# Optimization experiments

Hardware: AMD Instinct MI355X
Metric: run time of the kernel (lower is better)

## Reference

```python
import jax, jax.numpy as jnp
import numpy as np

D = 256; NH = 8; DH = D // NH; NL = 4; NP = 4; DFFN = 1024
SPATIAL = [(128, 128), (64, 64), (32, 32), (16, 16)]
LEN_IN = sum(h * w for h, w in SPATIAL)
N, LQ = 8, 1000


def _ln(x, g, b, eps=1e-5):
    m = jnp.mean(x, -1, keepdims=True)
    v = jnp.mean((x - m) ** 2, -1, keepdims=True)
    return (x - m) * jax.lax.rsqrt(v + eps) * g + b


def _ms_deform_core(value, loc, attn_w):
    # value (N,Len_in,NH,DH); loc (N,Lq,NH,NL,NP,2) in [0,1]; attn_w (N,Lq,NH,NL,NP)
    n, lq = loc.shape[0], loc.shape[1]
    out = jnp.zeros((n, NH, lq, DH), value.dtype)
    start = 0
    for l, (Hl, Wl) in enumerate(SPATIAL):
        v = value[:, start:start + Hl * Wl].transpose(0, 2, 1, 3)  # (N,NH,HW,DH)
        start += Hl * Wl
        # grid_sample-style mapping, align_corners=False, zero padding
        x = loc[:, :, :, l, :, 0] * Wl - 0.5  # (N,Lq,NH,NP)
        y = loc[:, :, :, l, :, 1] * Hl - 0.5
        x0 = jnp.floor(x); y0 = jnp.floor(y)
        lx = x - x0; ly = y - y0
        x0i = x0.astype(jnp.int32); y0i = y0.astype(jnp.int32)
        acc = jnp.zeros((n, NH, lq, NP, DH), value.dtype)
        for dy, dx, w in ((0, 0, (1 - ly) * (1 - lx)), (0, 1, (1 - ly) * lx),
                          (1, 0, ly * (1 - lx)), (1, 1, ly * lx)):
            xi = x0i + dx; yi = y0i + dy
            valid = ((xi >= 0) & (xi < Wl) & (yi >= 0) & (yi < Hl)).astype(value.dtype)
            idx = jnp.clip(yi, 0, Hl - 1) * Wl + jnp.clip(xi, 0, Wl - 1)  # (N,Lq,NH,NP)
            idx = idx.transpose(0, 2, 1, 3).reshape(n, NH, lq * NP)
            g = jnp.take_along_axis(v, idx[..., None], axis=2).reshape(n, NH, lq, NP, DH)
            acc = acc + g * (w * valid).transpose(0, 2, 1, 3)[..., None]
        out = out + jnp.sum(acc * attn_w[:, :, :, l].transpose(0, 2, 1, 3)[..., None], axis=3)
    return out.transpose(0, 2, 1, 3).reshape(n, lq, D)


def setup_inputs() -> dict:
    key = jax.random.key(0)
    ks = jax.random.split(key, 16)
    s = 0.02
    inp = {
        'tgt': jax.random.normal(ks[0], (N, LQ, D), jnp.float32),
        'query_pos': jax.random.normal(ks[1], (N, LQ, D), jnp.float32),
        'reference_points': jax.random.uniform(ks[2], (N, LQ, NL, 2), jnp.float32),
        'src': jax.random.normal(ks[3], (N, LEN_IN, D), jnp.float32),
        'spatial_shapes': jnp.array(SPATIAL, jnp.int32),
        'level_start_index': jnp.array(np.cumsum([0] + [h * w for h, w in SPATIAL[:-1]]), jnp.int32),
        # self-attention
        'sa_in_w': jax.random.normal(ks[4], (3 * D, D), jnp.float32) * s,
        'sa_in_b': jnp.zeros((3 * D,), jnp.float32),
        'sa_out_w': jax.random.normal(ks[5], (D, D), jnp.float32) * s,
        'sa_out_b': jnp.zeros((D,), jnp.float32),
        'norm2_g': jnp.ones((D,), jnp.float32), 'norm2_b': jnp.zeros((D,), jnp.float32),
        # MSDeformAttn
        'off_w': jax.random.normal(ks[6], (NH * NL * NP * 2, D), jnp.float32) * s,
        'off_b': jax.random.normal(ks[7], (NH * NL * NP * 2,), jnp.float32) * s,
        'aw_w': jax.random.normal(ks[8], (NH * NL * NP, D), jnp.float32) * s,
        'aw_b': jnp.zeros((NH * NL * NP,), jnp.float32),
        'val_w': jax.random.normal(ks[9], (D, D), jnp.float32) * s,
        'val_b': jnp.zeros((D,), jnp.float32),
        'outp_w': jax.random.normal(ks[10], (D, D), jnp.float32) * s,
        'outp_b': jnp.zeros((D,), jnp.float32),
        'norm1_g': jnp.ones((D,), jnp.float32), 'norm1_b': jnp.zeros((D,), jnp.float32),
        # FFN
        'ffn_w1': jax.random.normal(ks[11], (DFFN, D), jnp.float32) * s,
        'ffn_b1': jnp.zeros((DFFN,), jnp.float32),
        'ffn_w2': jax.random.normal(ks[12], (D, DFFN), jnp.float32) * s,
        'ffn_b2': jnp.zeros((D,), jnp.float32),
        'norm3_g': jnp.ones((D,), jnp.float32), 'norm3_b': jnp.zeros((D,), jnp.float32),
    }
    return inp


def reference(tgt, query_pos, reference_points, src, spatial_shapes, level_start_index,
              sa_in_w, sa_in_b, sa_out_w, sa_out_b, norm2_g, norm2_b,
              off_w, off_b, aw_w, aw_b, val_w, val_b, outp_w, outp_b, norm1_g, norm1_b,
              ffn_w1, ffn_b1, ffn_w2, ffn_b2, norm3_g, norm3_b):
    n, lq, _ = tgt.shape
    # ---- self-attention (q = k = tgt + pos, v = tgt), eval mode (dropout off)
    qk = tgt + query_pos
    wq, wk, wv = sa_in_w[:D], sa_in_w[D:2 * D], sa_in_w[2 * D:]
    bq, bk, bv = sa_in_b[:D], sa_in_b[D:2 * D], sa_in_b[2 * D:]
    q = (qk @ wq.T + bq).reshape(n, lq, NH, DH)
    k = (qk @ wk.T + bk).reshape(n, lq, NH, DH)
    v = (tgt @ wv.T + bv).reshape(n, lq, NH, DH)
    scores = jnp.einsum('bqhd,bkhd->bhqk', q, k) / np.sqrt(DH).astype(np.float32)
    attn = jax.nn.softmax(scores, axis=-1)
    sa = jnp.einsum('bhqk,bkhd->bqhd', attn, v).reshape(n, lq, D) @ sa_out_w.T + sa_out_b
    tgt = _ln(tgt + sa, norm2_g, norm2_b)
    # ---- multi-scale deformable cross-attention
    query = tgt + query_pos
    value = (src @ val_w.T + val_b).reshape(n, LEN_IN, NH, DH)
    offsets = (query @ off_w.T + off_b).reshape(n, lq, NH, NL, NP, 2)
    aw = (query @ aw_w.T + aw_b).reshape(n, lq, NH, NL * NP)
    aw = jax.nn.softmax(aw, axis=-1).reshape(n, lq, NH, NL, NP)
    # offset normalizer: (W_l, H_l)
    norm = jnp.stack([spatial_shapes[:, 1], spatial_shapes[:, 0]], -1).astype(tgt.dtype)
    loc = reference_points[:, :, None, :, None, :] + offsets / norm[None, None, None, :, None, :]
    ca = _ms_deform_core(value, loc, aw) @ outp_w.T + outp_b
    tgt = _ln(tgt + ca, norm1_g, norm1_b)
    # ---- FFN
    ff = jax.nn.relu(tgt @ ffn_w1.T + ffn_b1) @ ffn_w2.T + ffn_b2
    tgt = _ln(tgt + ff, norm3_g, norm3_b)
    return tgt
```

## Files before the change

kernel.cpp:

```cpp
#include <hip/hip_runtime.h>
#include <hip/hip_bf16.h>

#define D 256
#define NH 8
#define DH 32
#define NL 4
#define NP 4
#define DFFN 1024
#define LEN_IN 21760
#define NB 8
#define LQ 1000

typedef __hip_bfloat16 bf16;
typedef __attribute__((ext_vector_type(8))) short s8v;
typedef __attribute__((ext_vector_type(4))) float f4v;

template <typename T> __device__ inline T fromF(float x);
template <> __device__ inline float fromF<float>(float x) { return x; }
template <> __device__ inline bf16 fromF<bf16>(float x) { return __float2bfloat16(x); }

__device__ inline short bfr(float f) {
    unsigned u = __float_as_uint(f);
    u += 0x7fff + ((u >> 16) & 1);
    return (short)(u >> 16);
}
__device__ inline s8v pack8(float4 x, float4 y) {
    s8v r;
    r[0] = bfr(x.x); r[1] = bfr(x.y); r[2] = bfr(x.z); r[3] = bfr(x.w);
    r[4] = bfr(y.x); r[5] = bfr(y.y); r[6] = bfr(y.z); r[7] = bfr(y.w);
    return r;
}

__device__ inline unsigned cvtpk(float a, float b) {
    unsigned r;
    asm("v_cvt_pk_bf16_f32 %0, %1, %2" : "=v"(r) : "v"(a), "v"(b));
    return r;
}
__device__ inline s8v pkcvt8(float4 a, float4 b) {
    union { s8v v; unsigned u[4]; } r;
    r.u[0] = cvtpk(a.x, a.y);
    r.u[1] = cvtpk(a.z, a.w);
    r.u[2] = cvtpk(b.x, b.y);
    r.u[3] = cvtpk(b.z, b.w);
    return r.v;
}

__device__ __forceinline__ void gload_lds16(const void* gsrc, void* ldst) {
    __builtin_amdgcn_global_load_lds(
        (const __attribute__((address_space(1))) unsigned int*)gsrc,
        (__attribute__((address_space(3))) unsigned int*)ldst,
        16, 0, 0);
}

__global__ __launch_bounds__(256) void pack_weights(const float* __restrict__ s0, const float* __restrict__ s1,
                                                    const float* __restrict__ s2, const float* __restrict__ s3,
                                                    const float* __restrict__ s4, const float* __restrict__ s5,
                                                    const float* __restrict__ s6, const float* __restrict__ s7,
                                                    bf16* __restrict__ dst) {
    int g = blockIdx.x * 256 + threadIdx.x;
    const float* s; int base;
    if      (g <  49152) { s = s0; base = 0;      }
    else if (g <  65536) { s = s1; base = 49152;  }
    else if (g <  81920) { s = s2; base = 65536;  }
    else if (g <  90112) { s = s3; base = 81920;  }
    else if (g < 106496) { s = s4; base = 90112;  }
    else if (g < 122880) { s = s5; base = 106496; }
    else if (g < 188416) { s = s6; base = 122880; }
    else                 { s = s7; base = 188416; }
    float4 v = ((const float4*)s)[g - base];
    short4 o; o.x = bfr(v.x); o.y = bfr(v.y); o.z = bfr(v.z); o.w = bfr(v.w);
    ((short4*)dst)[g] = o;
}

__global__ __launch_bounds__(256) void add_f4(const float4* __restrict__ a, const float4* __restrict__ b,
                                              float4* __restrict__ o) {
    int i = blockIdx.x * 256 + threadIdx.x;
    float4 x = a[i], y = b[i];
    x.x += y.x; x.y += y.y; x.z += y.z; x.w += y.w;
    o[i] = x;
}

template <typename TA, typename TC, int R, int KK>
__global__ __launch_bounds__(256) void gemm_ldsA(const TA* __restrict__ A, const bf16* __restrict__ W,
                                                 const float* __restrict__ bias, TC* __restrict__ C,
                                                 int N, int do_relu) {
    constexpr int RB = KK * sizeof(TA);
    constexpr int LDSB = R * RB;
    constexpr int NSLOT = LDSB / 4096;
    constexpr int MI = R / 16;
    __shared__ char As[LDSB];

    const int tid = threadIdx.x;
    const int lane = tid & 63, wave = tid >> 6;
    const int fr = lane & 15, fq = lane >> 4;
    const int m0 = blockIdx.y * R;
    const int wn = blockIdx.x * 256 + wave * 64;

#pragma unroll
    for (int i = 0; i < NSLOT; ++i) {
        int s = i * 4096 + tid * 16;
        int r = s / RB;
        int c = (s % RB) ^ ((r & 7) << 4);
        const char* gsrc = (const char*)A + (size_t)(m0 + r) * RB + c;
        gload_lds16(gsrc, As + i * 4096 + tid * 16);
    }

    const bf16* wp[4];
#pragma unroll
    for (int j = 0; j < 4; ++j) wp[j] = W + (size_t)(wn + j * 16 + fr) * KK + fq * 8;

    f4v acc[MI][4];
#pragma unroll
    for (int i = 0; i < MI; ++i)
#pragma unroll
        for (int j = 0; j < 4; ++j) acc[i][j] = (f4v){0.f, 0.f, 0.f, 0.f};

    __syncthreads();

    auto step = [&](int kk) {
        s8v bfv[4];
#pragma unroll
        for (int j = 0; j < 4; ++j) bfv[j] = *(const s8v*)(wp[j] + kk * 32);
        s8v af[MI];
#pragma unroll
        for (int i = 0; i < MI; ++i) {
            const int row = i * 16 + fr;
            const int sw = (fr & 7) << 4;
            if constexpr (sizeof(TA) == 2) {
                int c0 = (kk * 64 + fq * 16) ^ sw;
                af[i] = *(const s8v*)(As + row * RB + c0);
            } else {
                int c0 = (kk * 128 + fq * 32) ^ sw;
                int c1 = (kk * 128 + fq * 32 + 16) ^ sw;
                float4 x0 = *(const float4*)(As + row * RB + c0);
                float4 x1 = *(const float4*)(As + row * RB + c1);
                af[i] = pkcvt8(x0, x1);
            }
        }
#pragma unroll
        for (int i = 0; i < MI; ++i)
#pragma unroll
            for (int j = 0; j < 4; ++j)
                acc[i][j] = __builtin_amdgcn_mfma_f32_16x16x32_bf16(af[i], bfv[j], acc[i][j], 0, 0, 0);
    };

    if constexpr (KK <= 256) {
#pragma unroll
        for (int kk = 0; kk < KK / 32; ++kk) step(kk);
    } else {
#pragma unroll 4
        for (int kk = 0; kk < KK / 32; ++kk) step(kk);
    }

#pragma unroll
    for (int j = 0; j < 4; ++j) {
        const int col = wn + j * 16 + fr;
        const float bb = bias[col];
#pragma unroll
        for (int i = 0; i < MI; ++i) {
            const int rbase = m0 + i * 16 + fq * 4;
#pragma unroll
            for (int r = 0; r < 4; ++r) {
                float v = acc[i][j][r] + bb;
                if (do_relu) v = fmaxf(v, 0.f);
                C[(size_t)(rbase + r) * N + col] = fromF<TC>(v);
            }
        }
    }
}

template <typename TA, typename TC, int MT, bool ADD2, int KK>
__global__ __launch_bounds__(256) void gemm_direct(const TA* __restrict__ A, const float* __restrict__ A2,
                                                   const bf16* __restrict__ W, const float* __restrict__ bias,
                                                   TC* __restrict__ C, int N, int do_relu) {
    const int tid = threadIdx.x;
    const int lane = tid & 63, wave = tid >> 6;
    const int fr = lane & 15, fq = lane >> 4;
    const int n0 = blockIdx.x * 128;
    const int wrow = blockIdx.y * (MT * 32) + (wave >> 1) * (MT * 16);
    const int wn = n0 + (wave & 1) * 64;

    const TA* ap[MT];
    const float* a2p[MT];
#pragma unroll
    for (int i = 0; i < MT; ++i) {
        size_t r = (size_t)(wrow + i * 16 + fr);
        ap[i] = A + r * KK + fq * 8;
        if constexpr (ADD2) a2p[i] = A2 + r * KK + fq * 8;
    }
    const bf16* wp[4];
#pragma unroll
    for (int j = 0; j < 4; ++j) wp[j] = W + (size_t)(wn + j * 16 + fr) * KK + fq * 8;

    f4v acc[MT][4];
#pragma unroll
    for (int i = 0; i < MT; ++i)
#pragma unroll
        for (int j = 0; j < 4; ++j) acc[i][j] = (f4v){0.f, 0.f, 0.f, 0.f};

    auto step = [&](int k0) {
        s8v bfv[4];
#pragma unroll
        for (int j = 0; j < 4; ++j) bfv[j] = *(const s8v*)(wp[j] + k0);
        s8v af[MT];
#pragma unroll
        for (int i = 0; i < MT; ++i) {
            if constexpr (sizeof(TA) == 2) {
                af[i] = *(const s8v*)((const bf16*)ap[i] + k0);
            } else {
                float4 x0 = *(const float4*)((const float*)ap[i] + k0);
                float4 x1 = *(const float4*)((const float*)ap[i] + k0 + 4);
                if constexpr (ADD2) {
                    float4 y0 = *(const float4*)(a2p[i] + k0);
                    float4 y1 = *(const float4*)(a2p[i] + k0 + 4);
                    x0.x += y0.x; x0.y += y0.y; x0.z += y0.z; x0.w += y0.w;
                    x1.x += y1.x; x1.y += y1.y; x1.z += y1.z; x1.w += y1.w;
                }
                af[i] = pkcvt8(x0, x1);
            }
        }
#pragma unroll
        for (int i = 0; i < MT; ++i)
#pragma unroll
            for (int j = 0; j < 4; ++j)
                acc[i][j] = __builtin_amdgcn_mfma_f32_16x16x32_bf16(af[i], bfv[j], acc[i][j], 0, 0, 0);
    };

#pragma unroll
    for (int k0 = 0; k0 < KK; k0 += 32) step(k0);

#pragma unroll
    for (int j = 0; j < 4; ++j) {
        const int col = wn + j * 16 + fr;
        const float bb = bias[col];
#pragma unroll
        for (int i = 0; i < MT; ++i) {
            const int rbase = wrow + i * 16 + fq * 4;
#pragma unroll
            for (int r = 0; r < 4; ++r) {
                float v = acc[i][j][r] + bb;
                if (do_relu) v = fmaxf(v, 0.f);
                C[(size_t)(rbase + r) * N + col] = fromF<TC>(v);
            }
        }
    }
}

__global__ __launch_bounds__(256) void attn_mfma(const float* __restrict__ q, const float* __restrict__ k,
                                                 const float* __restrict__ v, float* __restrict__ out) {
    const int h = blockIdx.y, n = blockIdx.z;
    const int tid = threadIdx.x, wave = tid >> 6, lane = tid & 63;
    const int fr = lane & 15, fq = lane >> 4;
    __shared__ short Ks[32 * 40];
    __shared__ short Vt[32 * 40];
    __shared__ short Pl[4][16 * 40];
    const int q0 = blockIdx.x * 64 + wave * 16;

    s8v qfrag;
    {
        int qr = q0 + fr; if (qr >= LQ) qr = LQ - 1;
        const float* qp = q + ((size_t)(n * LQ + qr)) * D + h * DH + fq * 8;
        float4 t0 = *(const float4*)qp;
        float4 t1 = *(const float4*)(qp + 4);
        const float sc = 0.17677669529663687f;
        t0.x *= sc; t0.y *= sc; t0.z *= sc; t0.w *= sc;
        t1.x *= sc; t1.y *= sc; t1.z *= sc; t1.w *= sc;
        qfrag = pack8(t0, t1);
    }

    f4v O0 = {0.f, 0.f, 0.f, 0.f}, O1 = {0.f, 0.f, 0.f, 0.f};
    float mrow[4] = {-1e30f, -1e30f, -1e30f, -1e30f};
    float lrow[4] = {0.f, 0.f, 0.f, 0.f};

    for (int kt = 0; kt < LQ; kt += 32) {
        __syncthreads();
        {
            int key = tid >> 3, d4 = (tid & 7) * 4;
            int gk = kt + key; if (gk >= LQ) gk = LQ - 1;
            const float* kp = k + ((size_t)(n * LQ + gk)) * D + h * DH + d4;
            float4 t = *(const float4*)kp;
            short4 pk; pk.x = bfr(t.x); pk.y = bfr(t.y); pk.z = bfr(t.z); pk.w = bfr(t.w);
            *(short4*)&Ks[key * 40 + d4] = pk;
        }
        {
            int d = tid & 31, key0 = (tid >> 5) * 4;
            float vv[4];
#pragma unroll
            for (int i = 0; i < 4; ++i) {
                int gk = kt + key0 + i; if (gk >= LQ) gk = LQ - 1;
                vv[i] = v[((size_t)(n * LQ + gk)) * D + h * DH + d];
            }
            short4 pk; pk.x = bfr(vv[0]); pk.y = bfr(vv[1]); pk.z = bfr(vv[2]); pk.w = bfr(vv[3]);
            *(short4*)&Vt[d * 40 + key0] = pk;
        }
        __syncthreads();

        f4v s0 = {0.f, 0.f, 0.f, 0.f}, s1 = {0.f, 0.f, 0.f, 0.f};
        s8v kf0 = *(s8v*)&Ks[fr * 40 + fq * 8];
        s8v kf1 = *(s8v*)&Ks[(16 + fr) * 40 + fq * 8];
        s0 = __builtin_amdgcn_mfma_f32_16x16x32_bf16(qfrag, kf0, s0, 0, 0, 0);
        s1 = __builtin_amdgcn_mfma_f32_16x16x32_bf16(qfrag, kf1, s1, 0, 0, 0);
        const bool val0 = (kt + fr) < LQ, val1 = (kt + 16 + fr) < LQ;

        float p0[4], p1[4], alpha[4];
#pragma unroll
        for (int r = 0; r < 4; ++r) {
            float a = val0 ? s0[r] : -1e30f;
            float b = val1 ? s1[r] : -1e30f;
            float mx = fmaxf(a, b);
            mx = fmaxf(mx, __shfl_xor(mx, 1, 64));
            mx = fmaxf(mx, __shfl_xor(mx, 2, 64));
            mx = fmaxf(mx, __shfl_xor(mx, 4, 64));
            mx = fmaxf(mx, __shfl_xor(mx, 8, 64));
            float mnew = fmaxf(mrow[r], mx);
            float al = __expf(mrow[r] - mnew);
            float e0 = __expf(a - mnew);
            float e1 = __expf(b - mnew);
            float ps = e0 + e1;
            ps += __shfl_xor(ps, 1, 64);
            ps += __shfl_xor(ps, 2, 64);
            ps += __shfl_xor(ps, 4, 64);
            ps += __shfl_xor(ps, 8, 64);
            lrow[r] = lrow[r] * al + ps;
            mrow[r] = mnew;
            alpha[r] = al;
            p0[r] = e0; p1[r] = e1;
        }

        short* pw = Pl[wave];
#pragma unroll
        for (int r = 0; r < 4; ++r) {
            pw[(fq * 4 + r) * 40 + fr] = bfr(p0[r]);
            pw[(fq * 4 + r) * 40 + 16 + fr] = bfr(p1[r]);
        }
        __builtin_amdgcn_s_waitcnt(0);
        s8v pfrag = *(s8v*)&pw[fr * 40 + fq * 8];
        s8v vf0 = *(s8v*)&Vt[fr * 40 + fq * 8];
        s8v vf1 = *(s8v*)&Vt[(16 + fr) * 40 + fq * 8];
#pragma unroll
        for (int r = 0; r < 4; ++r) { O0[r] *= alpha[r]; O1[r] *= alpha[r]; }
        O0 = __builtin_amdgcn_mfma_f32_16x16x32_bf16(pfrag, vf0, O0, 0, 0, 0);
        O1 = __builtin_amdgcn_mfma_f32_16x16x32_bf16(pfrag, vf1, O1, 0, 0, 0);
    }

#pragma unroll
    for (int r = 0; r < 4; ++r) {
        int qrow = q0 + fq * 4 + r;
        if (qrow < LQ) {
            float inv = 1.0f / lrow[r];
            float* op = out + ((size_t)(n * LQ + qrow)) * D + h * DH;
            op[fr] = O0[r] * inv;
            op[16 + fr] = O1[r] * inv;
        }
    }
}

__global__ __launch_bounds__(256) void ln_res_kernel(const float* __restrict__ base, const float* __restrict__ delta,
                                                     const float* __restrict__ g, const float* __restrict__ b,
                                                     float* __restrict__ out) {
    __shared__ float scratch[8];
    const size_t row = blockIdx.x;
    const int d = threadIdx.x;
    float x = base[row * D + d] + delta[row * D + d];
    float s1 = x, s2 = x * x;
    for (int o = 32; o > 0; o >>= 1) {
        s1 += __shfl_down(s1, o, 64);
        s2 += __shfl_down(s2, o, 64);
    }
    const int w = threadIdx.x >> 6, lane = threadIdx.x & 63;
    if (lane == 0) { scratch[w] = s1; scratch[4 + w] = s2; }
    __syncthreads();
    s1 = scratch[0] + scratch[1] + scratch[2] + scratch[3];
    s2 = scratch[4] + scratch[5] + scratch[6] + scratch[7];
    float mean = s1 * (1.0f / 256.0f);
    float var = s2 * (1.0f / 256.0f) - mean * mean;
    float rstd = rsqrtf(var + 1e-5f);
    float y = (x - mean) * rstd * g[d] + b[d];
    out[row * D + d] = y;
}

__global__ __launch_bounds__(256) void aw_softmax_kernel(float* __restrict__ aw, int ngrp) {
    int t = blockIdx.x * 256 + threadIdx.x;
    if (t >= ngrp) return;
    float* p = aw + (size_t)t * 16;
    float m = p[0];
#pragma unroll
    for (int i = 1; i < 16; ++i) m = fmaxf(m, p[i]);
    float s = 0.f;
    float e[16];
#pragma unroll
    for (int i = 0; i < 16; ++i) { e[i] = __expf(p[i] - m); s += e[i]; }
    float inv = 1.0f / s;
#pragma unroll
    for (int i = 0; i < 16; ++i) p[i] = e[i] * inv;
}

__global__ __launch_bounds__(256) void deform_kernel(const bf16* __restrict__ value, const float* __restrict__ offs,
                                                     const float* __restrict__ aw, const float* __restrict__ refp,
                                                     float* __restrict__ out) {
    const int h = blockIdx.y, n = blockIdx.z;
    const int tid = threadIdx.x;
    const int wave = tid >> 6, lane = tid & 63;
    const int qi = blockIdx.x * 4 + wave;
    const int c = lane & 15;
    const int l = lane >> 4;
    const size_t row = (size_t)n * LQ + qi;
    const int W = 128 >> l, H = 128 >> l;
    const int START[4] = {0, 16384, 20480, 21504};
    const float invW = 1.0f / W, invH = 1.0f / H;

    const float rx = refp[(row * NL + l) * 2 + 0];
    const float ry = refp[(row * NL + l) * 2 + 1];
    const bf16* vbase = value + ((size_t)n * LEN_IN + START[l]) * D + h * DH + 2 * c;
    const float* offp = offs + row * D + (h * NL + l) * NP * 2;
    const float* awp = aw + row * 128 + h * 16 + l * 4;

    float acc0 = 0.f, acc1 = 0.f;
#pragma unroll
    for (int p = 0; p < 4; ++p) {
        float ox = offp[p * 2 + 0];
        float oy = offp[p * 2 + 1];
        float wa = awp[p];
        float x = (rx + ox * invW) * W - 0.5f;
        float y = (ry + oy * invH) * H - 0.5f;
        float xf = floorf(x), yf = floorf(y);
        float lx = x - xf, ly = y - yf;
        int x0 = (int)xf, y0 = (int)yf;
        int x1 = x0 + 1, y1 = y0 + 1;
        float vx0 = (x0 >= 0 && x0 < W) ? 1.f : 0.f;
        float vx1 = (x1 >= 0 && x1 < W) ? 1.f : 0.f;
        float vy0 = (y0 >= 0 && y0 < H) ? 1.f : 0.f;
        float vy1 = (y1 >= 0 && y1 < H) ? 1.f : 0.f;
        int x0c = min(max(x0, 0), W - 1), x1c = min(max(x1, 0), W - 1);
        int y0c = min(max(y0, 0), H - 1), y1c = min(max(y1, 0), H - 1);
        float w00 = wa * (1.f - ly) * (1.f - lx) * vy0 * vx0;
        float w01 = wa * (1.f - ly) * lx * vy0 * vx1;
        float w10 = wa * ly * (1.f - lx) * vy1 * vx0;
        float w11 = wa * ly * lx * vy1 * vx1;
        unsigned u00 = *(const unsigned*)(vbase + (size_t)(y0c * W + x0c) * D);
        unsigned u01 = *(const unsigned*)(vbase + (size_t)(y0c * W + x1c) * D);
        unsigned u10 = *(const unsigned*)(vbase + (size_t)(y1c * W + x0c) * D);
        unsigned u11 = *(const unsigned*)(vbase + (size_t)(y1c * W + x1c) * D);
        acc0 += w00 * __uint_as_float(u00 << 16) + w01 * __uint_as_float(u01 << 16)
              + w10 * __uint_as_float(u10 << 16) + w11 * __uint_as_float(u11 << 16);
        acc1 += w00 * __uint_as_float(u00 & 0xffff0000u) + w01 * __uint_as_float(u01 & 0xffff0000u)
              + w10 * __uint_as_float(u10 & 0xffff0000u) + w11 * __uint_as_float(u11 & 0xffff0000u);
    }
    acc0 += __shfl_xor(acc0, 16, 64); acc0 += __shfl_xor(acc0, 32, 64);
    acc1 += __shfl_xor(acc1, 16, 64); acc1 += __shfl_xor(acc1, 32, 64);
    if (l == 0) {
        float2 st = {acc0, acc1};
        *(float2*)(out + row * D + h * DH + 2 * c) = st;
    }
}

extern "C" void kernel_launch(void* const* d_in, const int* in_sizes, int n_in,
                              void* d_out, int out_size, void* d_ws, size_t ws_size,
                              hipStream_t stream) {
    const float* tgt = (const float*)d_in[0];
    const float* qpos = (const float*)d_in[1];
    const float* refp = (const float*)d_in[2];
    const float* src = (const float*)d_in[3];
    const float* sa_in_w = (const float*)d_in[6];
    const float* sa_in_b = (const float*)d_in[7];
    const float* sa_out_w = (const float*)d_in[8];
    const float* sa_out_b = (const float*)d_in[9];
    const float* norm2_g = (const float*)d_in[10];
    const float* norm2_b = (const float*)d_in[11];
    const float* off_w = (const float*)d_in[12];
    const float* off_b = (const float*)d_in[13];
    const float* aw_w = (const float*)d_in[14];
    const float* aw_b = (const float*)d_in[15];
    const float* val_w = (const float*)d_in[16];
    const float* val_b = (const float*)d_in[17];
    const float* outp_w = (const float*)d_in[18];
    const float* outp_b = (const float*)d_in[19];
    const float* norm1_g = (const float*)d_in[20];
    const float* norm1_b = (const float*)d_in[21];
    const float* ffn_w1 = (const float*)d_in[22];
    const float* ffn_b1 = (const float*)d_in[23];
    const float* ffn_w2 = (const float*)d_in[24];
    const float* ffn_b2 = (const float*)d_in[25];
    const float* norm3_g = (const float*)d_in[26];
    const float* norm3_b = (const float*)d_in[27];
    float* outp = (float*)d_out;

    const size_t NTOK = (size_t)NB * LQ;
    const size_t NE = NTOK * D;
    float* w = (float*)d_ws;
    size_t off = 0;
    auto alloc = [&](size_t n) { float* p = w + off; off += n; return p; };
    float* bufA = alloc(NE);
    float* bufB = alloc(NE);
    float* bufC = alloc(NE);
    float* bufD = alloc(NE);
    float* tgt2 = alloc(NE);
    float* tgt3 = alloc(NE);
    float* awb = alloc(NTOK * 128);
    bf16* mid = (bf16*)alloc(NTOK * DFFN / 2);
    bf16* value = (bf16*)alloc((size_t)NB * LEN_IN * D / 2);
    bf16* wb = (bf16*)alloc(507904);

    const bf16* wq    = wb;
    const bf16* wk    = wb + 65536;
    const bf16* wv    = wb + 131072;
    const bf16* wo    = wb + 196608;
    const bf16* woff  = wb + 262144;
    const bf16* waw   = wb + 327680;
    const bf16* wval  = wb + 360448;
    const bf16* woutp = wb + 425984;
    const bf16* wf1   = wb + 491520;
    const bf16* wf2   = wb + 753664;

    const int M8K = (int)NTOK;
    dim3 g16(1, M8K / 16);
    dim3 gf1(DFFN / 256, M8K / 16);
    dim3 gVal(1, (NB * LEN_IN) / 32);
    dim3 gAw(1, M8K / 64);

    pack_weights<<<992, 256, 0, stream>>>(sa_in_w, sa_out_w, off_w, aw_w, val_w, outp_w, ffn_w1, ffn_w2, wb);

    add_f4<<<2000, 256, 0, stream>>>((const float4*)tgt, (const float4*)qpos, (float4*)bufA);
    gemm_ldsA<float, float, 16, 256><<<g16, 256, 0, stream>>>(bufA, wq, sa_in_b, bufB, D, 0);
    gemm_ldsA<float, float, 16, 256><<<g16, 256, 0, stream>>>(bufA, wk, sa_in_b + 256, bufC, D, 0);
    gemm_ldsA<float, float, 16, 256><<<g16, 256, 0, stream>>>(tgt, wv, sa_in_b + 512, bufD, D, 0);
    attn_mfma<<<dim3((LQ + 63) / 64, NH, NB), 256, 0, stream>>>(bufB, bufC, bufD, bufA);
    gemm_ldsA<float, float, 16, 256><<<g16, 256, 0, stream>>>(bufA, wo, sa_out_b, bufB, D, 0);
    ln_res_kernel<<<NTOK, 256, 0, stream>>>(tgt, bufB, norm2_g, norm2_b, tgt2);

    gemm_ldsA<float, bf16, 32, 256><<<gVal, 256, 0, stream>>>(src, wval, val_b, value, D, 0);
    add_f4<<<2000, 256, 0, stream>>>((const float4*)tgt2, (const float4*)qpos, (float4*)bufA);
    gemm_ldsA<float, float, 16, 256><<<g16, 256, 0, stream>>>(bufA, woff, off_b, bufD, D, 0);
    gemm_direct<float, float, 2, false, 256><<<gAw, 256, 0, stream>>>(bufA, nullptr, waw, aw_b, awb, 128, 0);
    aw_softmax_kernel<<<(int)(NTOK * NH + 255) / 256, 256, 0, stream>>>(awb, (int)(NTOK * NH));
    deform_kernel<<<dim3(LQ / 4, NH, NB), 256, 0, stream>>>(value, bufD, awb, refp, bufA);
    gemm_ldsA<float, float, 16, 256><<<g16, 256, 0, stream>>>(bufA, woutp, outp_b, bufB, D, 0);
    ln_res_kernel<<<NTOK, 256, 0, stream>>>(tgt2, bufB, norm1_g, norm1_b, tgt3);

    gemm_ldsA<float, bf16, 16, 256><<<gf1, 256, 0, stream>>>(tgt3, wf1, ffn_b1, mid, DFFN, 1);
    gemm_ldsA<bf16, float, 16, 1024><<<g16, 256, 0, stream>>>(mid, wf2, ffn_b2, bufC, D, 0);
    ln_res_kernel<<<NTOK, 256, 0, stream>>>(tgt3, bufC, norm3_g, norm3_b, outp);
}
```

Baseline: 687.1 us.

## Fuse Q/K and offset/attn-weight projections, add pipelined value-projection GEMM

Merges the Q and K projections into one GEMM producing a 512-wide buffer, and likewise fuses the sampling-offset and attention-weight projections into one 512-wide GEMM with concatenated (zero-padded) bias. Downstream attention, softmax and deform kernels are re-indexed to read from the interleaved buffers. The large value projection over src gets a dedicated 128x128-tile GEMM with double-buffered async global-to-LDS staging of A, XOR-swizzled LDS layout, and prefetched weight fragments. The fusions cut launches and reuse A-row reads. The new value GEMM targets the largest GEMM's memory/compute efficiency at the cost of more LDS per block. The aw GEMM now computes 128 wasted padded columns.

```diff
diff --git a/kernel.cpp b/kernel.cpp
--- a/kernel.cpp
+++ b/kernel.cpp
@@ -80,6 +80,15 @@
     o[i] = x;
 }
 
+__global__ __launch_bounds__(256) void bias_cat(const float* __restrict__ ob, const float* __restrict__ ab,
+                                                float* __restrict__ dst) {
+    int i = blockIdx.x * 256 + threadIdx.x;
+    float v = 0.f;
+    if (i < 256) v = ob[i];
+    else if (i < 384) v = ab[i - 256];
+    dst[i] = v;
+}
+
 template <typename TA, typename TC, int R, int KK>
 __global__ __launch_bounds__(256) void gemm_ldsA(const TA* __restrict__ A, const bf16* __restrict__ W,
                                                  const float* __restrict__ bias, TC* __restrict__ C,
@@ -169,85 +178,98 @@
     }
 }
 
-template <typename TA, typename TC, int MT, bool ADD2, int KK>
-__global__ __launch_bounds__(256) void gemm_direct(const TA* __restrict__ A, const float* __restrict__ A2,
-                                                   const bf16* __restrict__ W, const float* __restrict__ bias,
-                                                   TC* __restrict__ C, int N, int do_relu) {
+__global__ __launch_bounds__(256) void gemm_val(const float* __restrict__ A, const bf16* __restrict__ W,
+                                                const float* __restrict__ bias, bf16* __restrict__ C) {
+    __shared__ float As[2][4096];
     const int tid = threadIdx.x;
     const int lane = tid & 63, wave = tid >> 6;
     const int fr = lane & 15, fq = lane >> 4;
-    const int n0 = blockIdx.x * 128;
-    const int wrow = blockIdx.y * (MT * 32) + (wave >> 1) * (MT * 16);
-    const int wn = n0 + (wave & 1) * 64;
-
-    const TA* ap[MT];
-    const float* a2p[MT];
-#pragma unroll
-    for (int i = 0; i < MT; ++i) {
-        size_t r = (size_t)(wrow + i * 16 + fr);
-        ap[i] = A + r * KK + fq * 8;
-        if constexpr (ADD2) a2p[i] = A2 + r * KK + fq * 8;
+    const int m0 = blockIdx.y * 128;
+    const int wm = (wave >> 1) * 64;
+    const int wn = blockIdx.x * 128 + (wave & 1) * 64;
+
+    int srow[4], soff[4];
+#pragma unroll
+    for (int g = 0; g < 4; ++g) {
+        int s = g * 4096 + tid * 16;
+        int r = s >> 7;
+        srow[g] = r;
+        soff[g] = (s & 127) ^ ((r & 7) << 4);
+    }
+    int rb[4][2];
+#pragma unroll
+    for (int i = 0; i < 4; ++i) {
+        int r2 = wm + i * 16 + fr;
+        rb[i][0] = r2 * 128 + ((fq * 32) ^ ((r2 & 7) << 4));
+        rb[i][1] = r2 * 128 + ((fq * 32 + 16) ^ ((r2 & 7) << 4));
     }
     const bf16* wp[4];
 #pragma unroll
-    for (int j = 0; j < 4; ++j) wp[j] = W + (size_t)(wn + j * 16 + fr) * KK + fq * 8;
-
-    f4v acc[MT][4];
-#pragma unroll
-    for (int i = 0; i < MT; ++i)
+    for (int j = 0; j < 4; ++j) wp[j] = W + (size_t)(wn + j * 16 + fr) * 256 + fq * 8;
+
+    f4v acc[4][4];
+#pragma unroll
+    for (int i = 0; i < 4; ++i)
 #pragma unroll
         for (int j = 0; j < 4; ++j) acc[i][j] = (f4v){0.f, 0.f, 0.f, 0.f};
 
-    auto step = [&](int k0) {
-        s8v bfv[4];
-#pragma unroll
-        for (int j = 0; j < 4; ++j) bfv[j] = *(const s8v*)(wp[j] + k0);
-        s8v af[MT];
-#pragma unroll
-        for (int i = 0; i < MT; ++i) {
-            if constexpr (sizeof(TA) == 2) {
-                af[i] = *(const s8v*)((const bf16*)ap[i] + k0);
-            } else {
-                float4 x0 = *(const float4*)((const float*)ap[i] + k0);
-                float4 x1 = *(const float4*)((const float*)ap[i] + k0 + 4);
-                if constexpr (ADD2) {
-                    float4 y0 = *(const float4*)(a2p[i] + k0);
-                    float4 y1 = *(const float4*)(a2p[i] + k0 + 4);
-                    x0.x += y0.x; x0.y += y0.y; x0.z += y0.z; x0.w += y0.w;
-                    x1.x += y1.x; x1.y += y1.y; x1.z += y1.z; x1.w += y1.w;
-                }
-                af[i] = pkcvt8(x0, x1);
-            }
-        }
-#pragma unroll
-        for (int i = 0; i < MT; ++i)
+    auto stage = [&](int buf, int k0) {
+#pragma unroll
+        for (int g = 0; g < 4; ++g) {
+            const char* gsrc = (const char*)(A + (size_t)(m0 + srow[g]) * 256 + k0) + soff[g];
+            gload_lds16(gsrc, (char*)As[buf] + g * 4096 + tid * 16);
+        }
+    };
+
+    stage(0, 0);
+    s8v wcur[4], wnxt[4];
+#pragma unroll
+    for (int j = 0; j < 4; ++j) wcur[j] = *(const s8v*)wp[j];
+    __syncthreads();
+
+#pragma unroll
+    for (int kk = 0; kk < 8; ++kk) {
+        const int cur = kk & 1;
+        if (kk < 7) {
+            stage(cur ^ 1, (kk + 1) * 32);
+#pragma unroll
+            for (int j = 0; j < 4; ++j) wnxt[j] = *(const s8v*)(wp[j] + (kk + 1) * 32);
+        }
+        s8v af[4];
+#pragma unroll
+        for (int i = 0; i < 4; ++i) {
+            float4 x0 = *(const float4*)((const char*)As[cur] + rb[i][0]);
+            float4 x1 = *(const float4*)((const char*)As[cur] + rb[i][1]);
+            af[i] = pkcvt8(x0, x1);
+        }
+#pragma unroll
+        for (int i = 0; i < 4; ++i)
 #pragma unroll
             for (int j = 0; j < 4; ++j)
-                acc[i][j] = __builtin_amdgcn_mfma_f32_16x16x32_bf16(af[i], bfv[j], acc[i][j], 0, 0, 0);
-    };
-
-#pragma unroll
-    for (int k0 = 0; k0 < KK; k0 += 32) step(k0);
+                acc[i][j] = __builtin_amdgcn_mfma_f32_16x16x32_bf16(af[i], wcur[j], acc[i][j], 0, 0, 0);
+#pragma unroll
+        for (int j = 0; j < 4; ++j) wcur[j] = wnxt[j];
+        if (kk < 7) __syncthreads();
+    }
 
 #pragma unroll
     for (int j = 0; j < 4; ++j) {
         const int col = wn + j * 16 + fr;
         const float bb = bias[col];
 #pragma unroll
-        for (int i = 0; i < MT; ++i) {
-            const int rbase = wrow + i * 16 + fq * 4;
+        for (int i = 0; i < 4; ++i) {
+            const int rbase = m0 + wm + i * 16 + fq * 4;
 #pragma unroll
             for (int r = 0; r < 4; ++r) {
                 float v = acc[i][j][r] + bb;
-                if (do_relu) v = fmaxf(v, 0.f);
-                C[(size_t)(rbase + r) * N + col] = fromF<TC>(v);
+                C[(size_t)(rbase + r) * 256 + col] = fromF<bf16>(v);
             }
         }
     }
 }
 
-__global__ __launch_bounds__(256) void attn_mfma(const float* __restrict__ q, const float* __restrict__ k,
-                                                 const float* __restrict__ v, float* __restrict__ out) {
+__global__ __launch_bounds__(256) void attn_mfma(const float* __restrict__ qk, const float* __restrict__ v,
+                                                 float* __restrict__ out) {
     const int h = blockIdx.y, n = blockIdx.z;
     const int tid = threadIdx.x, wave = tid >> 6, lane = tid & 63;
     const int fr = lane & 15, fq = lane >> 4;
@@ -259,7 +281,7 @@
     s8v qfrag;
     {
         int qr = q0 + fr; if (qr >= LQ) qr = LQ - 1;
-        const float* qp = q + ((size_t)(n * LQ + qr)) * D + h * DH + fq * 8;
+        const float* qp = qk + ((size_t)(n * LQ + qr)) * 512 + h * DH + fq * 8;
         float4 t0 = *(const float4*)qp;
         float4 t1 = *(const float4*)(qp + 4);
         const float sc = 0.17677669529663687f;
@@ -277,7 +299,7 @@
         {
             int key = tid >> 3, d4 = (tid & 7) * 4;
             int gk = kt + key; if (gk >= LQ) gk = LQ - 1;
-            const float* kp = k + ((size_t)(n * LQ + gk)) * D + h * DH + d4;
+            const float* kp = qk + ((size_t)(n * LQ + gk)) * 512 + 256 + h * DH + d4;
             float4 t = *(const float4*)kp;
             short4 pk; pk.x = bfr(t.x); pk.y = bfr(t.y); pk.z = bfr(t.z); pk.w = bfr(t.w);
             *(short4*)&Ks[key * 40 + d4] = pk;
@@ -382,7 +404,7 @@
 __global__ __launch_bounds__(256) void aw_softmax_kernel(float* __restrict__ aw, int ngrp) {
     int t = blockIdx.x * 256 + threadIdx.x;
     if (t >= ngrp) return;
-    float* p = aw + (size_t)t * 16;
+    float* p = aw + (size_t)(t >> 3) * 512 + 256 + (t & 7) * 16;
     float m = p[0];
 #pragma unroll
     for (int i = 1; i < 16; ++i) m = fmaxf(m, p[i]);
@@ -395,9 +417,8 @@
     for (int i = 0; i < 16; ++i) p[i] = e[i] * inv;
 }
 
-__global__ __launch_bounds__(256) void deform_kernel(const bf16* __restrict__ value, const float* __restrict__ offs,
-                                                     const float* __restrict__ aw, const float* __restrict__ refp,
-                                                     float* __restrict__ out) {
+__global__ __launch_bounds__(256) void deform_kernel(const bf16* __restrict__ value, const float* __restrict__ offaw,
+                                                     const float* __restrict__ refp, float* __restrict__ out) {
     const int h = blockIdx.y, n = blockIdx.z;
     const int tid = threadIdx.x;
     const int wave = tid >> 6, lane = tid & 63;
@@ -412,8 +433,8 @@
     const float rx = refp[(row * NL + l) * 2 + 0];
     const float ry = refp[(row * NL + l) * 2 + 1];
     const bf16* vbase = value + ((size_t)n * LEN_IN + START[l]) * D + h * DH + 2 * c;
-    const float* offp = offs + row * D + (h * NL + l) * NP * 2;
-    const float* awp = aw + row * 128 + h * 16 + l * 4;
+    const float* offp = offaw + row * 512 + (h * NL + l) * NP * 2;
+    const float* awp = offaw + row * 512 + 256 + h * 16 + l * 4;
 
     float acc0 = 0.f, acc1 = 0.f;
 #pragma unroll
@@ -496,48 +517,48 @@
     float* bufD = alloc(NE);
     float* tgt2 = alloc(NE);
     float* tgt3 = alloc(NE);
-    float* awb = alloc(NTOK * 128);
+    float* biasoa = alloc(512);
     bf16* mid = (bf16*)alloc(NTOK * DFFN / 2);
     bf16* value = (bf16*)alloc((size_t)NB * LEN_IN * D / 2);
     bf16* wb = (bf16*)alloc(507904);
 
-    const bf16* wq    = wb;
-    const bf16* wk    = wb + 65536;
+    float* qkbuf = bufB;
+    float* offaw = bufC;
+
+    const bf16* wqk   = wb;
     const bf16* wv    = wb + 131072;
     const bf16* wo    = wb + 196608;
     const bf16* woff  = wb + 262144;
-    const bf16* waw   = wb + 327680;
     const bf16* wval  = wb + 360448;
     const bf16* woutp = wb + 425984;
     const bf16* wf1   = wb + 491520;
     const bf16* wf2   = wb + 753664;
 
     const int M8K = (int)NTOK;
-    dim3 g16(1, M8K / 16);
+    dim3 g16x1(1, M8K / 16);
+    dim3 g16x2(2, M8K / 16);
     dim3 gf1(DFFN / 256, M8K / 16);
-    dim3 gVal(1, (NB * LEN_IN) / 32);
-    dim3 gAw(1, M8K / 64);
+    dim3 gVal(2, (NB * LEN_IN) / 128);
 
     pack_weights<<<992, 256, 0, stream>>>(sa_in_w, sa_out_w, off_w, aw_w, val_w, outp_w, ffn_w1, ffn_w2, wb);
+    bias_cat<<<2, 256, 0, stream>>>(off_b, aw_b, biasoa);
 
     add_f4<<<2000, 256, 0, stream>>>((const float4*)tgt, (const float4*)qpos, (float4*)bufA);
-    gemm_ldsA<float, float, 16, 256><<<g16, 256, 0, stream>>>(bufA, wq, sa_in_b, bufB, D, 0);
-    gemm_ldsA<float, float, 16, 256><<<g16, 256, 0, stream>>>(bufA, wk, sa_in_b + 256, bufC, D, 0);
-    gemm_ldsA<float, float, 16, 256><<<g16, 256, 0, stream>>>(tgt, wv, sa_in_b + 512, bufD, D, 0);
-    attn_mfma<<<dim3((LQ + 63) / 64, NH, NB), 256, 0, stream>>>(bufB, bufC, bufD, bufA);
-    gemm_ldsA<float, float, 16, 256><<<g16, 256, 0, stream>>>(bufA, wo, sa_out_b, bufB, D, 0);
+    gemm_ldsA<float, float, 16, 256><<<g16x2, 256, 0, stream>>>(bufA, wqk, sa_in_b, qkbuf, 512, 0);
+    gemm_ldsA<float, float, 16, 256><<<g16x1, 256, 0, stream>>>(tgt, wv, sa_in_b + 512, bufD, D, 0);
+    attn_mfma<<<dim3((LQ + 63) / 64, NH, NB), 256, 0, stream>>>(qkbuf, bufD, bufA);
+    gemm_ldsA<float, float, 16, 256><<<g16x1, 256, 0, stream>>>(bufA, wo, sa_out_b, bufB, D, 0);
     ln_res_kernel<<<NTOK, 256, 0, stream>>>(tgt, bufB, norm2_g, norm2_b, tgt2);
 
-    gemm_ldsA<float, bf16, 32, 256><<<gVal, 256, 0, stream>>>(src, wval, val_b, value, D, 0);
+    gemm_val<<<gVal, 256, 0, stream>>>(src, wval, val_b, value);
     add_f4<<<2000, 256, 0, stream>>>((const float4*)tgt2, (const float4*)qpos, (float4*)bufA);
-    gemm_ldsA<float, float, 16, 256><<<g16, 256, 0, stream>>>(bufA, woff, off_b, bufD, D, 0);
-    gemm_direct<float, float, 2, false, 256><<<gAw, 256, 0, stream>>>(bufA, nullptr, waw, aw_b, awb, 128, 0);
-    aw_softmax_kernel<<<(int)(NTOK * NH + 255) / 256, 256, 0, stream>>>(awb, (int)(NTOK * NH));
-    deform_kernel<<<dim3(LQ / 4, NH, NB), 256, 0, stream>>>(value, bufD, awb, refp, bufA);
-    gemm_ldsA<float, float, 16, 256><<<g16, 256, 0, stream>>>(bufA, woutp, outp_b, bufB, D, 0);
+    gemm_ldsA<float, float, 16, 256><<<g16x2, 256, 0, stream>>>(bufA, woff, biasoa, offaw, 512, 0);
+    aw_softmax_kernel<<<(int)(NTOK * NH + 255) / 256, 256, 0, stream>>>(offaw, (int)(NTOK * NH));
+    deform_kernel<<<dim3(LQ / 4, NH, NB), 256, 0, stream>>>(value, offaw, refp, bufA);
+    gemm_ldsA<float, float, 16, 256><<<g16x1, 256, 0, stream>>>(bufA, woutp, outp_b, bufB, D, 0);
     ln_res_kernel<<<NTOK, 256, 0, stream>>>(tgt2, bufB, norm1_g, norm1_b, tgt3);
 
     gemm_ldsA<float, bf16, 16, 256><<<gf1, 256, 0, stream>>>(tgt3, wf1, ffn_b1, mid, DFFN, 1);
-    gemm_ldsA<bf16, float, 16, 1024><<<g16, 256, 0, stream>>>(mid, wf2, ffn_b2, bufC, D, 0);
+    gemm_ldsA<bf16, float, 16, 1024><<<g16x1, 256, 0, stream>>>(mid, wf2, ffn_b2, bufC, D, 0);
     ln_res_kernel<<<NTOK, 256, 0, stream>>>(tgt3, bufC, norm3_g, norm3_b, outp);
 }
```

Result: faster. 652.2 us (-5.1%).
